# Performance work log

Measured on AMD Instinct MI355X. Metric: run time of the kernel, lower is better.

The kernel has to match this reference:

```python
import jax, jax.numpy as jnp
import numpy as np

D = 256; FF = 1024; NH = 8; NL = 4; NP = 4; DH = D // NH
SHAPES = [(64, 64), (32, 32), (16, 16), (8, 8)]
B = 4; N = sum(h * w for h, w in SHAPES)


def _ln(x, g, b, eps=1e-5):
    m = jnp.mean(x, -1, keepdims=True)
    v = jnp.var(x, -1, keepdims=True)
    return (x - m) * jax.lax.rsqrt(v + eps) * g + b


def _bilinear(v, x, y, H, W):
    # v: [B, H*W, nh, dh]; x, y: [B, Nq, nh, P] pixel coords (grid_sample, align_corners=False, zero pad)
    x0 = jnp.floor(x); y0 = jnp.floor(y)
    fx = x - x0; fy = y - y0
    x0 = x0.astype(jnp.int32); y0 = y0.astype(jnp.int32)
    dh = v.shape[-1]
    acc = 0.0
    for xi, yi, w in ((x0, y0, (1 - fx) * (1 - fy)),
                      (x0 + 1, y0, fx * (1 - fy)),
                      (x0, y0 + 1, (1 - fx) * fy),
                      (x0 + 1, y0 + 1, fx * fy)):
        valid = ((xi >= 0) & (xi < W) & (yi >= 0) & (yi < H)).astype(v.dtype)
        idx = jnp.clip(yi, 0, H - 1) * W + jnp.clip(xi, 0, W - 1)  # [B,Nq,nh,P]
        Bq, Nq, nh, P = idx.shape
        idx2 = idx.transpose(0, 1, 3, 2).reshape(Bq, Nq * P, nh, 1)
        idx2 = jnp.broadcast_to(idx2, (Bq, Nq * P, nh, dh))
        g = jnp.take_along_axis(v, idx2, axis=1)  # [B, Nq*P, nh, dh]
        g = g.reshape(Bq, Nq, P, nh, dh).transpose(0, 1, 3, 2, 4)  # [B,Nq,nh,P,dh]
        acc = acc + g * (w * valid)[..., None]
    return acc


def _msdeform(value, loc, attn, shapes):
    # value [B,N,nh,dh]; loc [B,Nq,nh,L,P,2] in [0,1]; attn [B,Nq,nh,L,P]
    out = 0.0; start = 0
    for l, (H, W) in enumerate(shapes):
        v = value[:, start:start + H * W]
        start += H * W
        x = loc[:, :, :, l, :, 0] * W - 0.5
        y = loc[:, :, :, l, :, 1] * H - 0.5
        s = _bilinear(v, x, y, H, W)  # [B,Nq,nh,P,dh]
        out = out + jnp.einsum('bqhpd,bqhp->bqhd', s, attn[:, :, :, l, :])
    return out


def _forward(src, pos, reference_points, w_value, b_value, w_off, b_off, w_attn, b_attn,
             w_out, b_out, g1, be1, w1, b1, w2, b2, g2, be2, padding_mask, shapes):
    q = src + pos
    value = src @ w_value.T + b_value
    value = jnp.where(padding_mask[..., None], 0.0, value).reshape(B, N, NH, DH)
    off = (q @ w_off.T + b_off).reshape(B, N, NH, NL, NP, 2)
    attn = jax.nn.softmax((q @ w_attn.T + b_attn).reshape(B, N, NH, NL * NP), axis=-1)
    attn = attn.reshape(B, N, NH, NL, NP)
    normalizer = jnp.array([[w, h] for h, w in shapes], jnp.float32)  # [L,2] as (W,H)
    loc = reference_points[:, :, None, :, None, :] + off / normalizer[None, None, None, :, None, :]
    a = _msdeform(value, loc, attn, shapes).reshape(B, N, D) @ w_out.T + b_out
    x = _ln(src + a, g1, be1)
    f = jax.nn.relu(x @ w1.T + b1) @ w2.T + b2
    return _ln(x + f, g2, be2)


def setup_inputs() -> dict:
    key = jax.random.key(0)
    ks = iter(jax.random.split(key, 24))
    def p(shape, scale=0.02):
        return jax.random.normal(next(ks), shape, jnp.float32) * scale
    d = {}
    d['src'] = jax.random.normal(next(ks), (B, N, D), jnp.float32)
    d['pos'] = jax.random.normal(next(ks), (B, N, D), jnp.float32)
    d['reference_points'] = jax.random.uniform(next(ks), (B, N, NL, 2), dtype=jnp.float32)
    d['w_value'] = p((D, D)); d['b_value'] = jnp.zeros((D,), jnp.float32)
    d['w_off'] = p((NH * NL * NP * 2, D), 0.001); d['b_off'] = p((NH * NL * NP * 2,), 0.1)
    d['w_attn'] = p((NH * NL * NP, D)); d['b_attn'] = jnp.zeros((NH * NL * NP,), jnp.float32)
    d['w_out'] = p((D, D)); d['b_out'] = jnp.zeros((D,), jnp.float32)
    d['g1'] = jnp.ones((D,), jnp.float32); d['be1'] = jnp.zeros((D,), jnp.float32)
    d['w1'] = p((FF, D)); d['b1'] = jnp.zeros((FF,), jnp.float32)
    d['w2'] = p((D, FF)); d['b2'] = jnp.zeros((D,), jnp.float32)
    d['g2'] = jnp.ones((D,), jnp.float32); d['be2'] = jnp.zeros((D,), jnp.float32)
    d['spatial_shapes'] = jnp.array(SHAPES, jnp.int32)
    d['level_start_index'] = jnp.array(np.cumsum([0] + [h * w for h, w in SHAPES[:-1]]), jnp.int32)
    d['padding_mask'] = jnp.zeros((B, N), bool)
    return d


def reference(src, pos, reference_points, w_value, b_value, w_off, b_off, w_attn, b_attn,
              w_out, b_out, g1, be1, w1, b1, w2, b2, g2, be2,
              spatial_shapes, level_start_index, padding_mask):
    shapes = [tuple(map(int, s)) for s in np.asarray(spatial_shapes)]  # static per-level shapes
    return _forward(src, pos, reference_points, w_value, b_value, w_off, b_off, w_attn, b_attn,
                    w_out, b_out, g1, be1, w1, b1, w2, b2, g2, be2, padding_mask, shapes)
```

## Files before the change

kernel.cpp:

```cpp
#include <hip/hip_runtime.h>

#define B_SZ   4
#define NTOK   5440
#define MTOT   (B_SZ*NTOK)
#define DMODEL 256
#define FFDIM  1024

typedef __attribute__((ext_vector_type(8))) __bf16 bf16x8;
typedef __attribute__((ext_vector_type(4))) float  f32x4;

static __device__ __forceinline__ unsigned short f2b(float f) {
    unsigned u = __builtin_bit_cast(unsigned, f);
    u = (u + 0x7FFF + ((u >> 16) & 1)) >> 16;
    return (unsigned short)u;
}
static __device__ __forceinline__ float b2f(unsigned short s) {
    return __builtin_bit_cast(float, (unsigned)s << 16);
}
static __device__ __forceinline__ float lo_bf(unsigned u) {
    return __builtin_bit_cast(float, u << 16);
}
static __device__ __forceinline__ float hi_bf(unsigned u) {
    return __builtin_bit_cast(float, u & 0xffff0000u);
}

#define GLL(gp, lp) __builtin_amdgcn_global_load_lds( \
    (const __attribute__((address_space(1))) void*)(gp), \
    (__attribute__((address_space(3))) void*)(lp), 16, 0, 0)

__global__ __launch_bounds__(256)
void qkv_gemm(const unsigned short* __restrict__ src_bf,
              const unsigned short* __restrict__ q_bf,
              const unsigned short* __restrict__ wv_b,
              const unsigned short* __restrict__ woa_b,
              const float* __restrict__ b_value,
              const float* __restrict__ b_off, const float* __restrict__ b_attn,
              const unsigned char* __restrict__ rowmask,
              unsigned short* __restrict__ value_b, unsigned short* __restrict__ oa_b)
{
    const int K = 256;
    const int y = blockIdx.y;
    const bool isv = (y < 2);
    const unsigned short* A  = isv ? src_bf : q_bf;
    const unsigned short* Wt = isv ? wv_b : woa_b;
    unsigned short* C = isv ? value_b : oa_b;
    const int ldc  = isv ? 256 : 384;
    const int col0 = (isv ? y : (y - 2)) * 128;

    __shared__ unsigned short As[128 * 32];
    __shared__ unsigned short Bs[128 * 32];
    const int tid  = threadIdx.x;
    const int lane = tid & 63;
    const int wave = tid >> 6;
    const int row0 = blockIdx.x * 128;
    const int wr = (wave >> 1) * 64, wc = (wave & 1) * 64;
    const int mrow = lane & 15, quad = lane >> 4;

    f32x4 acc[4][4] = {};
    const int ri0 = tid >> 2,            ki0 = (tid & 3) * 8;
    const int ri1 = (256 + tid) >> 2,    ki1 = ((256 + tid) & 3) * 8;
    const int lds0 = (wave * 64) * 8, lds1 = (256 + wave * 64) * 8;

    for (int k0 = 0; k0 < K; k0 += 32) {
        __syncthreads();
        GLL(A  + (size_t)(row0 + ri0) * K + k0 + ki0, &As[lds0]);
        GLL(Wt + (size_t)(col0 + ri0) * K + k0 + ki0, &Bs[lds0]);
        GLL(A  + (size_t)(row0 + ri1) * K + k0 + ki1, &As[lds1]);
        GLL(Wt + (size_t)(col0 + ri1) * K + k0 + ki1, &Bs[lds1]);
        __syncthreads();

        bf16x8 af[4], bfr[4];
        #pragma unroll
        for (int t4 = 0; t4 < 4; ++t4) {
            af[t4]  = *(const bf16x8*)&As[(wr + t4 * 16 + mrow) * 32 + quad * 8];
            bfr[t4] = *(const bf16x8*)&Bs[(wc + t4 * 16 + mrow) * 32 + quad * 8];
        }
        #pragma unroll
        for (int ti = 0; ti < 4; ++ti)
            #pragma unroll
            for (int tj = 0; tj < 4; ++tj)
                acc[ti][tj] = __builtin_amdgcn_mfma_f32_16x16x32_bf16(
                                  af[ti], bfr[tj], acc[ti][tj], 0, 0, 0);
    }

    #pragma unroll
    for (int tj = 0; tj < 4; ++tj) {
        const int col = col0 + wc + tj * 16 + mrow;
        const float bv = isv ? b_value[col] : (col < 256 ? b_off[col] : b_attn[col - 256]);
        #pragma unroll
        for (int ti = 0; ti < 4; ++ti)
            #pragma unroll
            for (int r = 0; r < 4; ++r) {
                const int row = row0 + wr + ti * 16 + quad * 4 + r;
                float v = acc[ti][tj][r] + bv;
                if (isv && rowmask[row]) v = 0.f;
                C[(size_t)row * ldc + col] = f2b(v);
            }
    }
}

__global__ __launch_bounds__(256)
void mfma_gemm(const unsigned short* __restrict__ A,
               const unsigned short* __restrict__ Wt,
               const float* __restrict__ bias,
               unsigned short* __restrict__ Cb,
               int M, int Nout, int K, int relu)
{
    __shared__ unsigned short As[128 * 32];
    __shared__ unsigned short Bs[128 * 32];
    const int tid  = threadIdx.x;
    const int lane = tid & 63;
    const int wave = tid >> 6;
    const int row0 = blockIdx.x * 128, col0 = blockIdx.y * 128;
    const int wr = (wave >> 1) * 64, wc = (wave & 1) * 64;
    const int mrow = lane & 15, quad = lane >> 4;

    f32x4 acc[4][4] = {};
    const int ri0 = tid >> 2,            ki0 = (tid & 3) * 8;
    const int ri1 = (256 + tid) >> 2,    ki1 = ((256 + tid) & 3) * 8;
    const int lds0 = (wave * 64) * 8, lds1 = (256 + wave * 64) * 8;

    for (int k0 = 0; k0 < K; k0 += 32) {
        __syncthreads();
        GLL(A  + (size_t)(row0 + ri0) * K + k0 + ki0, &As[lds0]);
        GLL(Wt + (size_t)(col0 + ri0) * K + k0 + ki0, &Bs[lds0]);
        GLL(A  + (size_t)(row0 + ri1) * K + k0 + ki1, &As[lds1]);
        GLL(Wt + (size_t)(col0 + ri1) * K + k0 + ki1, &Bs[lds1]);
        __syncthreads();

        bf16x8 af[4], bfr[4];
        #pragma unroll
        for (int t4 = 0; t4 < 4; ++t4) {
            af[t4]  = *(const bf16x8*)&As[(wr + t4 * 16 + mrow) * 32 + quad * 8];
            bfr[t4] = *(const bf16x8*)&Bs[(wc + t4 * 16 + mrow) * 32 + quad * 8];
        }
        #pragma unroll
        for (int ti = 0; ti < 4; ++ti)
            #pragma unroll
            for (int tj = 0; tj < 4; ++tj)
                acc[ti][tj] = __builtin_amdgcn_mfma_f32_16x16x32_bf16(
                                  af[ti], bfr[tj], acc[ti][tj], 0, 0, 0);
    }

    #pragma unroll
    for (int tj = 0; tj < 4; ++tj) {
        const int col = col0 + wc + tj * 16 + mrow;
        const float bv = bias[col];
        #pragma unroll
        for (int ti = 0; ti < 4; ++ti)
            #pragma unroll
            for (int r = 0; r < 4; ++r) {
                const int row = row0 + wr + ti * 16 + quad * 4 + r;
                float v = acc[ti][tj][r] + bv;
                if (relu) v = fmaxf(v, 0.f);
                Cb[(size_t)row * Nout + col] = f2b(v);
            }
    }
}

__global__ __launch_bounds__(256)
void gemm_ln(const unsigned short* __restrict__ A,
             const unsigned short* __restrict__ Wt,
             const float* __restrict__ bias,
             const float* __restrict__ resid,
             const float* __restrict__ g, const float* __restrict__ be,
             float* __restrict__ out_f, unsigned short* __restrict__ out_b,
             int K)
{
    __shared__ unsigned short As[64 * 32];
    __shared__ unsigned short Bs[256 * 32];
    __shared__ float s_red[64][8];

    const int tid  = threadIdx.x;
    const int lane = tid & 63;
    const int wave = tid >> 6;
    const int row0 = blockIdx.x * 64;
    const int mrow = lane & 15, quad = lane >> 4;
    const int colw = wave * 64;

    f32x4 acc[4][4] = {};
    const int ri = tid >> 2, ki = (tid & 3) * 8;

    for (int k0 = 0; k0 < K; k0 += 32) {
        __syncthreads();
        GLL(A + (size_t)(row0 + ri) * K + k0 + ki, &As[(wave * 64) * 8]);
        #pragma unroll
        for (int i = 0; i < 4; ++i)
            GLL(Wt + (size_t)(i * 64 + ri) * K + k0 + ki, &Bs[(i * 256 + wave * 64) * 8]);
        __syncthreads();

        bf16x8 af[4], bfr[4];
        #pragma unroll
        for (int t4 = 0; t4 < 4; ++t4) {
            af[t4]  = *(const bf16x8*)&As[(t4 * 16 + mrow) * 32 + quad * 8];
            bfr[t4] = *(const bf16x8*)&Bs[(colw + t4 * 16 + mrow) * 32 + quad * 8];
        }
        #pragma unroll
        for (int ti = 0; ti < 4; ++ti)
            #pragma unroll
            for (int tj = 0; tj < 4; ++tj)
                acc[ti][tj] = __builtin_amdgcn_mfma_f32_16x16x32_bf16(
                                  af[ti], bfr[tj], acc[ti][tj], 0, 0, 0);
    }

    float bv[4], gv[4], bev[4];
    #pragma unroll
    for (int tj = 0; tj < 4; ++tj) {
        const int col = colw + tj * 16 + mrow;
        bv[tj] = bias[col]; gv[tj] = g[col]; bev[tj] = be[col];
    }

    __syncthreads();

    #pragma unroll
    for (int ti = 0; ti < 4; ++ti) {
        #pragma unroll
        for (int r = 0; r < 4; ++r) {
            const int row_local = ti * 16 + quad * 4 + r;
            const int row = row0 + row_local;
            float s = 0.f, sq = 0.f;
            #pragma unroll
            for (int tj = 0; tj < 4; ++tj) {
                const int col = colw + tj * 16 + mrow;
                float t = acc[ti][tj][r] + bv[tj] + resid[(size_t)row * 256 + col];
                acc[ti][tj][r] = t;
                s += t; sq += t * t;
            }
            #pragma unroll
            for (int m = 1; m < 16; m <<= 1) {
                s  += __shfl_xor(s, m, 64);
                sq += __shfl_xor(sq, m, 64);
            }
            if (mrow == 0) { s_red[row_local][wave] = s; s_red[row_local][4 + wave] = sq; }
        }
    }
    __syncthreads();

    #pragma unroll
    for (int ti = 0; ti < 4; ++ti) {
        #pragma unroll
        for (int r = 0; r < 4; ++r) {
            const int row_local = ti * 16 + quad * 4 + r;
            const int row = row0 + row_local;
            const float4 su = *(const float4*)&s_red[row_local][0];
            const float4 qu = *(const float4*)&s_red[row_local][4];
            const float mean = (su.x + su.y + su.z + su.w) * (1.f / 256.f);
            const float var  = (qu.x + qu.y + qu.z + qu.w) * (1.f / 256.f) - mean * mean;
            const float rstd = rsqrtf(var + 1e-5f);
            #pragma unroll
            for (int tj = 0; tj < 4; ++tj) {
                const int col = colw + tj * 16 + mrow;
                const float o = (acc[ti][tj][r] - mean) * rstd * gv[tj] + bev[tj];
                out_f[(size_t)row * 256 + col] = o;
                if (out_b) out_b[(size_t)row * 256 + col] = f2b(o);
            }
        }
    }
}

__global__ __launch_bounds__(256)
void sampling_kernel(const unsigned short* __restrict__ value,
                     const unsigned short* __restrict__ oa,
                     const float* __restrict__ refp,
                     unsigned short* __restrict__ samp)
{
    __shared__ int4 s_pk[4 * 264];
    const int t0  = blockIdx.x * 4;
    const int tid = threadIdx.x;

    #pragma unroll
    for (int rep = 0; rep < 2; ++rep) {
        const int e   = rep * 256 + tid;
        const int tok = e >> 7;
        const int hp  = e & 127;
        const int h   = hp >> 4, i16 = hp & 15, l = i16 >> 2;
        const int t   = t0 + tok;

        const float logit = b2f(oa[(size_t)t * 384 + 256 + h * 16 + i16]);
        float mx = logit;
        #pragma unroll
        for (int o = 8; o; o >>= 1) mx = fmaxf(mx, __shfl_xor(mx, o, 16));
        const float ex = __expf(logit - mx);
        float ssum = ex;
        #pragma unroll
        for (int o = 8; o; o >>= 1) ssum += __shfl_xor(ssum, o, 16);
        const float aw = ex / ssum;

        const int   Wl_t[4]   = {64, 32, 16, 8};
        const int   LSTB_t[4] = {0, 4096 * 512, 5120 * 512, 5376 * 512};
        const int   Wl   = Wl_t[l];
        const int   LSTB = LSTB_t[l];
        const float fW   = (float)Wl;

        const unsigned ov = *(const unsigned*)&oa[(size_t)t * 384 + h * 32 + i16 * 2];
        const float ox = lo_bf(ov), oy = hi_bf(ov);
        const float2 rxy = *(const float2*)&refp[(size_t)t * 8 + l * 2];
        const float x = rxy.x * fW + ox - 0.5f;
        const float y = rxy.y * fW + oy - 0.5f;
        const float x0 = floorf(x), y0 = floorf(y);
        const float fx = x - x0, fy = y - y0;
        const int   ix = (int)x0, iy = (int)y0;
        const bool  vx0 = (ix >= 0) & (ix < Wl), vx1 = (ix + 1 >= 0) & (ix + 1 < Wl);

        #pragma unroll
        for (int j = 0; j < 2; ++j) {
            const int  yv = iy + j;
            const bool vy = (yv >= 0) & (yv < Wl);
            const float wy = (j ? fy : 1.f - fy) * aw;
            const int  rowb = LSTB + yv * Wl * 512;
            const float w0 = (vy & vx0) ? wy * (1.f - fx) : 0.f;
            const float w1 = (vy & vx1) ? wy * fx : 0.f;
            const int  i0 = (vy & vx0) ? rowb + ix * 512 : 0;
            const int  i1 = (vy & vx1) ? rowb + (ix + 1) * 512 : 0;
            s_pk[tok * 264 + h * 33 + i16 * 2 + j] =
                make_int4(i0, __float_as_int(w0), i1, __float_as_int(w1));
        }
    }
    __syncthreads();

    const int wv_  = tid >> 6;
    const int lane = tid & 63;
    const int h    = lane >> 3, dq = lane & 7;
    const int t    = t0 + wv_;
    const int b    = t / NTOK;
    const char* vb = (const char*)value + ((size_t)b * NTOK * 256 + h * 32 + dq * 4) * 2;
    const int4* pk = s_pk + wv_ * 264 + h * 33;

    float a0 = 0.f, a1 = 0.f, a2 = 0.f, a3 = 0.f;
    #pragma unroll 8
    for (int i = 0; i < 32; ++i) {
        const int4 p = pk[i];
        const uint2 u0 = *(const uint2*)(vb + p.x);
        const uint2 u1 = *(const uint2*)(vb + p.z);
        const float w0 = __int_as_float(p.y), w1 = __int_as_float(p.w);
        a0 += lo_bf(u0.x) * w0; a1 += hi_bf(u0.x) * w0;
        a2 += lo_bf(u0.y) * w0; a3 += hi_bf(u0.y) * w0;
        a0 += lo_bf(u1.x) * w1; a1 += hi_bf(u1.x) * w1;
        a2 += lo_bf(u1.y) * w1; a3 += hi_bf(u1.y) * w1;
    }
    ushort4 o;
    o.x = f2b(a0); o.y = f2b(a1); o.z = f2b(a2); o.w = f2b(a3);
    *(ushort4*)(samp + (size_t)t * 256 + h * 32 + dq * 4) = o;
}

__global__ __launch_bounds__(256)
void prep_kernel(const float* __restrict__ src, const float* __restrict__ pos,
                 const float* __restrict__ wv, const float* __restrict__ woff,
                 const float* __restrict__ wattn, const float* __restrict__ wout,
                 const float* __restrict__ w1, const float* __restrict__ w2,
                 unsigned short* __restrict__ q_bf, unsigned short* __restrict__ src_bf,
                 unsigned short* __restrict__ wv_b, unsigned short* __restrict__ woa_b,
                 unsigned short* __restrict__ wout_b,
                 unsigned short* __restrict__ w1_b, unsigned short* __restrict__ w2_b)
{
    const int v = blockIdx.x * 256 + threadIdx.x;
    if (v < 1392640) {
        const float4 s = ((const float4*)src)[v];
        const float4 p = ((const float4*)pos)[v];
        ushort4 qo, so;
        qo.x = f2b(s.x + p.x); qo.y = f2b(s.y + p.y);
        qo.z = f2b(s.z + p.z); qo.w = f2b(s.w + p.w);
        so.x = f2b(s.x); so.y = f2b(s.y); so.z = f2b(s.z); so.w = f2b(s.w);
        ((ushort4*)q_bf)[v]   = qo;
        ((ushort4*)src_bf)[v] = so;
        return;
    }
    const int v2 = v - 1392640;
    const float* s; unsigned short* d; int off;
    if      (v2 <  16384) { s = wv;    d = wv_b;          off = v2; }
    else if (v2 <  32768) { s = woff;  d = woa_b;         off = v2 - 16384; }
    else if (v2 <  40960) { s = wattn; d = woa_b + 65536; off = v2 - 32768; }
    else if (v2 <  57344) { s = wout;  d = wout_b;        off = v2 - 40960; }
    else if (v2 < 122880) { s = w1;    d = w1_b;          off = v2 - 57344; }
    else                  { s = w2;    d = w2_b;          off = v2 - 122880; }
    const float4 f = ((const float4*)s)[off];
    ushort4 u; u.x = f2b(f.x); u.y = f2b(f.y); u.z = f2b(f.z); u.w = f2b(f.w);
    ((ushort4*)d)[off] = u;
}

extern "C" void kernel_launch(void* const* d_in, const int* in_sizes, int n_in,
                              void* d_out, int out_size, void* d_ws, size_t ws_size,
                              hipStream_t stream) {
    const float* src     = (const float*)d_in[0];
    const float* pos     = (const float*)d_in[1];
    const float* refp    = (const float*)d_in[2];
    const float* w_value = (const float*)d_in[3];
    const float* b_value = (const float*)d_in[4];
    const float* w_off   = (const float*)d_in[5];
    const float* b_off   = (const float*)d_in[6];
    const float* w_attn  = (const float*)d_in[7];
    const float* b_attn  = (const float*)d_in[8];
    const float* w_out   = (const float*)d_in[9];
    const float* b_out   = (const float*)d_in[10];
    const float* g1      = (const float*)d_in[11];
    const float* be1     = (const float*)d_in[12];
    const float* w1      = (const float*)d_in[13];
    const float* b1      = (const float*)d_in[14];
    const float* w2      = (const float*)d_in[15];
    const float* b2      = (const float*)d_in[16];
    const float* g2      = (const float*)d_in[17];
    const float* be2     = (const float*)d_in[18];
    const unsigned char* pmask = (const unsigned char*)d_in[21];

    char* ws = (char*)d_ws;
    const size_t SZ16 = (size_t)MTOT * 256 * 2;
    unsigned short* q_bf    = (unsigned short*)(ws);
    unsigned short* src_bf  = (unsigned short*)(ws + SZ16);
    unsigned short* value_b = (unsigned short*)(ws + 2 * SZ16);
    unsigned short* oa_b    = (unsigned short*)(ws + 3 * SZ16);
    unsigned short* samp    = (unsigned short*)(ws + 3 * SZ16 + SZ16 * 3 / 2);
    unsigned short* h_bf    = (unsigned short*)(ws + 5 * SZ16 + SZ16 * 3 / 2);
    unsigned short* wts     = (unsigned short*)(ws + 9 * SZ16 + SZ16 * 3 / 2);
    float*          x       = (float*)(ws);
    unsigned short* x_bf    = (unsigned short*)(ws + 2 * SZ16);

    unsigned short* wv_b    = wts;
    unsigned short* woa_b   = wv_b   + 65536;
    unsigned short* wout_b  = woa_b  + 98304;
    unsigned short* w1_b    = wout_b + 65536;
    unsigned short* w2_b    = w1_b   + 262144;

    const dim3 blk(256);

    prep_kernel<<<dim3(6176), blk, 0, stream>>>(src, pos, w_value, w_off, w_attn,
                                                w_out, w1, w2, q_bf, src_bf,
                                                wv_b, woa_b, wout_b, w1_b, w2_b);
    qkv_gemm<<<dim3(MTOT / 128, 5), blk, 0, stream>>>(
        src_bf, q_bf, wv_b, woa_b, b_value, b_off, b_attn, pmask, value_b, oa_b);
    sampling_kernel<<<dim3(MTOT / 4), blk, 0, stream>>>(value_b, oa_b, refp, samp);
    gemm_ln<<<dim3(MTOT / 64), blk, 0, stream>>>(
        samp, wout_b, b_out, src, g1, be1, x, x_bf, DMODEL);
    mfma_gemm<<<dim3(MTOT / 128, FFDIM / 128), blk, 0, stream>>>(
        x_bf, w1_b, b1, h_bf, MTOT, FFDIM, DMODEL, 1);
    gemm_ln<<<dim3(MTOT / 64), blk, 0, stream>>>(
        h_bf, w2_b, b2, x, g2, be2, (float*)d_out, nullptr, FFDIM);
}
```

Before: 292.9 us.

## Swap GEMM grid order, shrink gemm_ln tiles, repack sampling with prefetch

Several changes at once. The QKV and FFN GEMM grids are transposed so consecutive blocks share the same row tile, which is meant to improve cache reuse of activations. gemm_ln now uses 32-row tiles, doubling the block count for better occupancy. The sampling kernel packs each index and weight into one 32-bit word and uses 8 tokens per block with 16-byte loads and software prefetch. Softmax drops max subtraction, which risks overflow, and the bf16 weights lose precision.

```diff
diff --git a/kernel.cpp b/kernel.cpp
--- a/kernel.cpp
+++ b/kernel.cpp
@@ -39,7 +39,7 @@
               unsigned short* __restrict__ value_b, unsigned short* __restrict__ oa_b)
 {
     const int K = 256;
-    const int y = blockIdx.y;
+    const int y = blockIdx.x;
     const bool isv = (y < 2);
     const unsigned short* A  = isv ? src_bf : q_bf;
     const unsigned short* Wt = isv ? wv_b : woa_b;
@@ -52,7 +52,7 @@
     const int tid  = threadIdx.x;
     const int lane = tid & 63;
     const int wave = tid >> 6;
-    const int row0 = blockIdx.x * 128;
+    const int row0 = blockIdx.y * 128;
     const int wr = (wave >> 1) * 64, wc = (wave & 1) * 64;
     const int mrow = lane & 15, quad = lane >> 4;
 
@@ -111,7 +111,7 @@
     const int tid  = threadIdx.x;
     const int lane = tid & 63;
     const int wave = tid >> 6;
-    const int row0 = blockIdx.x * 128, col0 = blockIdx.y * 128;
+    const int row0 = blockIdx.y * 128, col0 = blockIdx.x * 128;
     const int wr = (wave >> 1) * 64, wc = (wave & 1) * 64;
     const int mrow = lane & 15, quad = lane >> 4;
 
@@ -167,36 +167,39 @@
              float* __restrict__ out_f, unsigned short* __restrict__ out_b,
              int K)
 {
-    __shared__ unsigned short As[64 * 32];
+    __shared__ unsigned short As[32 * 32];
     __shared__ unsigned short Bs[256 * 32];
-    __shared__ float s_red[64][8];
+    __shared__ float s_red[32][8];
 
     const int tid  = threadIdx.x;
     const int lane = tid & 63;
     const int wave = tid >> 6;
-    const int row0 = blockIdx.x * 64;
+    const int row0 = blockIdx.x * 32;
     const int mrow = lane & 15, quad = lane >> 4;
     const int colw = wave * 64;
 
-    f32x4 acc[4][4] = {};
+    f32x4 acc[2][4] = {};
     const int ri = tid >> 2, ki = (tid & 3) * 8;
 
     for (int k0 = 0; k0 < K; k0 += 32) {
         __syncthreads();
-        GLL(A + (size_t)(row0 + ri) * K + k0 + ki, &As[(wave * 64) * 8]);
-        #pragma unroll
-        for (int i = 0; i < 4; ++i)
-            GLL(Wt + (size_t)(i * 64 + ri) * K + k0 + ki, &Bs[(i * 256 + wave * 64) * 8]);
-        __syncthreads();
-
-        bf16x8 af[4], bfr[4];
-        #pragma unroll
-        for (int t4 = 0; t4 < 4; ++t4) {
-            af[t4]  = *(const bf16x8*)&As[(t4 * 16 + mrow) * 32 + quad * 8];
-            bfr[t4] = *(const bf16x8*)&Bs[(colw + t4 * 16 + mrow) * 32 + quad * 8];
-        }
-        #pragma unroll
-        for (int ti = 0; ti < 4; ++ti)
+        if (wave < 2)
+            GLL(A + (size_t)(row0 + ri) * K + k0 + ki, &As[(wave * 64) * 8]);
+        #pragma unroll
+        for (int rep = 0; rep < 4; ++rep)
+            GLL(Wt + (size_t)(rep * 64 + ri) * K + k0 + ki,
+                &Bs[(rep * 256 + wave * 64) * 8]);
+        __syncthreads();
+
+        bf16x8 af[2], bfr[4];
+        #pragma unroll
+        for (int ti = 0; ti < 2; ++ti)
+            af[ti] = *(const bf16x8*)&As[(ti * 16 + mrow) * 32 + quad * 8];
+        #pragma unroll
+        for (int tj = 0; tj < 4; ++tj)
+            bfr[tj] = *(const bf16x8*)&Bs[(colw + tj * 16 + mrow) * 32 + quad * 8];
+        #pragma unroll
+        for (int ti = 0; ti < 2; ++ti)
             #pragma unroll
             for (int tj = 0; tj < 4; ++tj)
                 acc[ti][tj] = __builtin_amdgcn_mfma_f32_16x16x32_bf16(
@@ -210,10 +213,8 @@
         bv[tj] = bias[col]; gv[tj] = g[col]; bev[tj] = be[col];
     }
 
-    __syncthreads();
-
-    #pragma unroll
-    for (int ti = 0; ti < 4; ++ti) {
+    #pragma unroll
+    for (int ti = 0; ti < 2; ++ti) {
         #pragma unroll
         for (int r = 0; r < 4; ++r) {
             const int row_local = ti * 16 + quad * 4 + r;
@@ -237,7 +238,7 @@
     __syncthreads();
 
     #pragma unroll
-    for (int ti = 0; ti < 4; ++ti) {
+    for (int ti = 0; ti < 2; ++ti) {
         #pragma unroll
         for (int r = 0; r < 4; ++r) {
             const int row_local = ti * 16 + quad * 4 + r;
@@ -264,33 +265,29 @@
                      const float* __restrict__ refp,
                      unsigned short* __restrict__ samp)
 {
-    __shared__ int4 s_pk[4 * 264];
-    const int t0  = blockIdx.x * 4;
+    __shared__ unsigned s_pk[64 * 68];
+    const int t0  = blockIdx.x * 8;
     const int tid = threadIdx.x;
 
     #pragma unroll
-    for (int rep = 0; rep < 2; ++rep) {
+    for (int rep = 0; rep < 4; ++rep) {
         const int e   = rep * 256 + tid;
         const int tok = e >> 7;
         const int hp  = e & 127;
         const int h   = hp >> 4, i16 = hp & 15, l = i16 >> 2;
         const int t   = t0 + tok;
 
-        const float logit = b2f(oa[(size_t)t * 384 + 256 + h * 16 + i16]);
-        float mx = logit;
-        #pragma unroll
-        for (int o = 8; o; o >>= 1) mx = fmaxf(mx, __shfl_xor(mx, o, 16));
-        const float ex = __expf(logit - mx);
+        const float ex = __expf(b2f(oa[(size_t)t * 384 + 256 + h * 16 + i16]));
         float ssum = ex;
         #pragma unroll
         for (int o = 8; o; o >>= 1) ssum += __shfl_xor(ssum, o, 16);
         const float aw = ex / ssum;
 
-        const int   Wl_t[4]   = {64, 32, 16, 8};
-        const int   LSTB_t[4] = {0, 4096 * 512, 5120 * 512, 5376 * 512};
-        const int   Wl   = Wl_t[l];
-        const int   LSTB = LSTB_t[l];
-        const float fW   = (float)Wl;
+        const int   Wl_t[4]  = {64, 32, 16, 8};
+        const int   LST_t[4] = {0, 4096, 5120, 5376};
+        const int   Wl  = Wl_t[l];
+        const int   LST = LST_t[l];
+        const float fW  = (float)Wl;
 
         const unsigned ov = *(const unsigned*)&oa[(size_t)t * 384 + h * 32 + i16 * 2];
         const float ox = lo_bf(ov), oy = hi_bf(ov);
@@ -302,45 +299,59 @@
         const int   ix = (int)x0, iy = (int)y0;
         const bool  vx0 = (ix >= 0) & (ix < Wl), vx1 = (ix + 1 >= 0) & (ix + 1 < Wl);
 
+        const int base = (tok * 8 + h) * 68 + i16 * 4;
         #pragma unroll
         for (int j = 0; j < 2; ++j) {
             const int  yv = iy + j;
             const bool vy = (yv >= 0) & (yv < Wl);
             const float wy = (j ? fy : 1.f - fy) * aw;
-            const int  rowb = LSTB + yv * Wl * 512;
+            const int  rowi = LST + yv * Wl;
             const float w0 = (vy & vx0) ? wy * (1.f - fx) : 0.f;
             const float w1 = (vy & vx1) ? wy * fx : 0.f;
-            const int  i0 = (vy & vx0) ? rowb + ix * 512 : 0;
-            const int  i1 = (vy & vx1) ? rowb + (ix + 1) * 512 : 0;
-            s_pk[tok * 264 + h * 33 + i16 * 2 + j] =
-                make_int4(i0, __float_as_int(w0), i1, __float_as_int(w1));
+            const unsigned i0 = (vy & vx0) ? (unsigned)(rowi + ix) : 0u;
+            const unsigned i1 = (vy & vx1) ? (unsigned)(rowi + ix + 1) : 0u;
+            s_pk[base + j * 2 + 0] = (i0 << 16) | f2b(w0);
+            s_pk[base + j * 2 + 1] = (i1 << 16) | f2b(w1);
         }
     }
     __syncthreads();
 
     const int wv_  = tid >> 6;
     const int lane = tid & 63;
-    const int h    = lane >> 3, dq = lane & 7;
-    const int t    = t0 + wv_;
+    const int t2   = lane >> 5;
+    const int h    = (lane >> 2) & 7;
+    const int dq   = lane & 3;
+    const int tok  = wv_ * 2 + t2;
+    const int t    = t0 + tok;
     const int b    = t / NTOK;
-    const char* vb = (const char*)value + ((size_t)b * NTOK * 256 + h * 32 + dq * 4) * 2;
-    const int4* pk = s_pk + wv_ * 264 + h * 33;
+    const char* vb = (const char*)value + ((size_t)b * NTOK * 256 + h * 32 + dq * 8) * 2;
+    const unsigned* sp = s_pk + (tok * 8 + h) * 68;
 
     float a0 = 0.f, a1 = 0.f, a2 = 0.f, a3 = 0.f;
+    float a4 = 0.f, a5 = 0.f, a6 = 0.f, a7 = 0.f;
+
+    unsigned pkc = sp[0];
+    uint4 vc = *(const uint4*)(vb + (size_t)(pkc >> 16) * 512);
     #pragma unroll 8
-    for (int i = 0; i < 32; ++i) {
-        const int4 p = pk[i];
-        const uint2 u0 = *(const uint2*)(vb + p.x);
-        const uint2 u1 = *(const uint2*)(vb + p.z);
-        const float w0 = __int_as_float(p.y), w1 = __int_as_float(p.w);
-        a0 += lo_bf(u0.x) * w0; a1 += hi_bf(u0.x) * w0;
-        a2 += lo_bf(u0.y) * w0; a3 += hi_bf(u0.y) * w0;
-        a0 += lo_bf(u1.x) * w1; a1 += hi_bf(u1.x) * w1;
-        a2 += lo_bf(u1.y) * w1; a3 += hi_bf(u1.y) * w1;
-    }
-    ushort4 o;
-    o.x = f2b(a0); o.y = f2b(a1); o.z = f2b(a2); o.w = f2b(a3);
-    *(ushort4*)(samp + (size_t)t * 256 + h * 32 + dq * 4) = o;
+    for (int i = 0; i < 64; ++i) {
+        unsigned pkn = 0; uint4 vn = make_uint4(0, 0, 0, 0);
+        if (i < 63) {
+            pkn = sp[i + 1];
+            vn = *(const uint4*)(vb + (size_t)(pkn >> 16) * 512);
+        }
+        const float w = lo_bf(pkc);
+        a0 += lo_bf(vc.x) * w; a1 += hi_bf(vc.x) * w;
+        a2 += lo_bf(vc.y) * w; a3 += hi_bf(vc.y) * w;
+        a4 += lo_bf(vc.z) * w; a5 += hi_bf(vc.z) * w;
+        a6 += lo_bf(vc.w) * w; a7 += hi_bf(vc.w) * w;
+        pkc = pkn; vc = vn;
+    }
+    ushort4 o0, o1;
+    o0.x = f2b(a0); o0.y = f2b(a1); o0.z = f2b(a2); o0.w = f2b(a3);
+    o1.x = f2b(a4); o1.y = f2b(a5); o1.z = f2b(a6); o1.w = f2b(a7);
+    unsigned short* op = samp + (size_t)t * 256 + h * 32 + dq * 8;
+    *(ushort4*)(op)     = o0;
+    *(ushort4*)(op + 4) = o1;
 }
 
 __global__ __launch_bounds__(256)
@@ -425,13 +436,13 @@
     prep_kernel<<<dim3(6176), blk, 0, stream>>>(src, pos, w_value, w_off, w_attn,
                                                 w_out, w1, w2, q_bf, src_bf,
                                                 wv_b, woa_b, wout_b, w1_b, w2_b);
-    qkv_gemm<<<dim3(MTOT / 128, 5), blk, 0, stream>>>(
+    qkv_gemm<<<dim3(5, MTOT / 128), blk, 0, stream>>>(
         src_bf, q_bf, wv_b, woa_b, b_value, b_off, b_attn, pmask, value_b, oa_b);
-    sampling_kernel<<<dim3(MTOT / 4), blk, 0, stream>>>(value_b, oa_b, refp, samp);
-    gemm_ln<<<dim3(MTOT / 64), blk, 0, stream>>>(
+    sampling_kernel<<<dim3(MTOT / 8), blk, 0, stream>>>(value_b, oa_b, refp, samp);
+    gemm_ln<<<dim3(MTOT / 32), blk, 0, stream>>>(
         samp, wout_b, b_out, src, g1, be1, x, x_bf, DMODEL);
-    mfma_gemm<<<dim3(MTOT / 128, FFDIM / 128), blk, 0, stream>>>(
+    mfma_gemm<<<dim3(FFDIM / 128, MTOT / 128), blk, 0, stream>>>(
         x_bf, w1_b, b1, h_bf, MTOT, FFDIM, DMODEL, 1);
-    gemm_ln<<<dim3(MTOT / 64), blk, 0, stream>>>(
+    gemm_ln<<<dim3(MTOT / 32), blk, 0, stream>>>(
         h_bf, w2_b, b2, x, g2, be2, (float*)d_out, nullptr, FFDIM);
 }
```

New measurement: 271.5 us. 1.08x faster.
